# Kernel tuning notes

Measured on AMD Instinct MI355X. Metric: run time of the kernel, lower is better.

## Reference

```python
import jax, jax.numpy as jnp
import numpy as np

N_NODES = 100_000
N_EDGES = 1_600_000
NODE_FEATURES = 22


def setup_inputs() -> dict:
    key = jax.random.key(0)
    ks = jax.random.split(key, 10)
    s = 0.1
    x = jax.random.normal(ks[0], (N_NODES, NODE_FEATURES), dtype=jnp.float32)
    edge_index = jax.random.randint(ks[1], (2, N_EDGES), 0, N_NODES, dtype=jnp.int64)
    return {
        "x": x,
        "edge_index": edge_index,
        "W_embed": jax.random.normal(ks[2], (NODE_FEATURES, 32), jnp.float32) * s,
        "b_embed": jax.random.normal(ks[3], (32,), jnp.float32) * s,
        "W1": jax.random.normal(ks[4], (32, 32), jnp.float32) * s,
        "b1": jax.random.normal(ks[5], (32,), jnp.float32) * s,
        "W2": jax.random.normal(ks[6], (64, 32), jnp.float32) * s,
        "b2": jax.random.normal(ks[7], (32,), jnp.float32) * s,
        "W_pred": jax.random.normal(ks[8], (64, 1), jnp.float32) * s,
        "b_pred": jax.random.normal(ks[9], (1,), jnp.float32) * s,
    }


def gcn_conv(h, src, dst, deg_inv_sqrt, W, b, num_nodes):
    """PyG GCNConv: h' = scatter_add(norm_ij * (h W)[src] -> dst) + b.
    src/dst already include self-loops; deg_inv_sqrt precomputed on dst."""
    h = h @ W  # [N, out]
    norm = deg_inv_sqrt[src] * deg_inv_sqrt[dst]  # [E]
    msg = h[src] * norm[:, None]  # gather + normalize
    out = jax.ops.segment_sum(msg, dst, num_segments=num_nodes)  # scatter-add
    return out + b


def reference(x, edge_index, W_embed, b_embed, W1, b1, W2, b2, W_pred, b_pred):
    n = x.shape[0]
    loop = jnp.arange(n, dtype=edge_index.dtype)
    src = jnp.concatenate([edge_index[0], loop])  # add self-loops
    dst = jnp.concatenate([edge_index[1], loop])
    deg = jax.ops.segment_sum(jnp.ones_like(src, dtype=x.dtype), dst, num_segments=n)
    deg_inv_sqrt = jnp.where(deg > 0, jax.lax.rsqrt(jnp.maximum(deg, 1.0)), 0.0)

    h = x @ W_embed + b_embed  # MLP_embed
    # dropout is identity at eval time
    h0 = h
    h = gcn_conv(h, src, dst, deg_inv_sqrt, W1, b1, n)
    h = jax.nn.relu(h)
    h = jnp.concatenate([h, h0], axis=1)  # [N, 64]
    h = gcn_conv(h, src, dst, deg_inv_sqrt, W2, b2, n)
    h = jax.nn.relu(h)
    h = jnp.concatenate([h, h0], axis=1)  # [N, 64]
    delta = h @ W_pred + b_pred  # [N, 1]
    out = jax.nn.relu(delta + x[:, 1:2])
    return out
```

## Files before the change

### kernel.cpp

```cpp
#include <hip/hip_runtime.h>
#include <hip/hip_bf16.h>

#define NF 22
#define H  32
#define BSH 8
#define CAP 8192
#define CHUNK 2048

__device__ __forceinline__ float bflo(unsigned int v) { return __uint_as_float(v << 16); }
__device__ __forceinline__ float bfhi(unsigned int v) { return __uint_as_float(v & 0xffff0000u); }

__global__ void init_cur(int* __restrict__ cursor, int NB) {
    int i = blockIdx.x * blockDim.x + threadIdx.x;
    if (i < NB) cursor[i] = i * CAP;
}

__global__ __launch_bounds__(256) void bin_edges(
    const int* __restrict__ src, const int* __restrict__ dst,
    int* __restrict__ cursor, int* __restrict__ binned, int E, int NB)
{
    __shared__ int lh[512];
    __shared__ int lcur[512];
    int tid = threadIdx.x;
    for (int j = tid; j < NB; j += 256) lh[j] = 0;
    __syncthreads();
    int e0 = blockIdx.x * CHUNK;
    int ee = min(e0 + CHUNK, E);
    for (int i = e0 + tid; i < ee; i += 256) atomicAdd(&lh[dst[i] >> BSH], 1);
    __syncthreads();
    for (int j = tid; j < NB; j += 256) {
        int c = lh[j];
        if (c) lcur[j] = atomicAdd(&cursor[j], c);
    }
    __syncthreads();
    for (int i = e0 + tid; i < ee; i += 256) {
        int d = dst[i];
        int p = atomicAdd(&lcur[d >> BSH], 1);
        binned[p] = (src[i] << BSH) | (d & 255);
    }
}

__global__ __launch_bounds__(1024) void bucket_csr(
    const int* __restrict__ cursor, const int* __restrict__ binned,
    int* __restrict__ rowptr, int* __restrict__ rowcnt, int* __restrict__ sorted_src,
    float* __restrict__ dis, int N)
{
    __shared__ int cnt[256];
    __shared__ int s[256];
    __shared__ int lcur[256];
    int b = blockIdx.x, tid = threadIdx.x;
    int bn = b << BSH;
    if (tid < 256) cnt[tid] = 0;
    __syncthreads();
    int es = b * CAP, ee = cursor[b];
    for (int i = es + tid; i < ee; i += 1024) atomicAdd(&cnt[binned[i] & 255], 1);
    __syncthreads();
    int v = 0;
    if (tid < 256) { v = cnt[tid]; s[tid] = v; }
    __syncthreads();
    for (int off = 1; off < 256; off <<= 1) {
        int t = 0;
        if (tid < 256 && tid >= off) t = s[tid - off];
        __syncthreads();
        if (tid < 256) s[tid] += t;
        __syncthreads();
    }
    if (tid < 256) {
        int ex = s[tid] - v;
        lcur[tid] = ex;
        int n = bn + tid;
        if (n < N) {
            rowptr[n] = es + ex;
            rowcnt[n] = v;
            dis[n] = rsqrtf((float)(v + 1));
        }
    }
    __syncthreads();
    for (int i = es + tid; i < ee; i += 1024) {
        int e = binned[i];
        int p = atomicAdd(&lcur[e & 255], 1);
        sorted_src[es + p] = e >> BSH;
    }
}

__global__ __launch_bounds__(256) void embed_g1(
    const float* __restrict__ x, const float* __restrict__ We,
    const float* __restrict__ be, const float* __restrict__ W1,
    const float* __restrict__ dis, float* __restrict__ h0,
    __hip_bfloat16* __restrict__ g, int N)
{
    __shared__ float sWe[NF * H];
    __shared__ float sW1[H * H];
    __shared__ float sbe[H];
    __shared__ float sx[8][NF];
    __shared__ float sh[8][H];

    int tid = threadIdx.x;
    for (int j = tid; j < NF * H; j += 256) sWe[j] = We[j];
    for (int j = tid; j < H * H; j += 256) sW1[j] = W1[j];
    if (tid < H) sbe[tid] = be[tid];

    int grp = tid >> 5, t = tid & 31;
    int node = blockIdx.x * 8 + grp;
    int nodec = node < N ? node : N - 1;
    if (t < NF) sx[grp][t] = x[(size_t)nodec * NF + t];
    __syncthreads();

    float h = sbe[t];
#pragma unroll
    for (int k = 0; k < NF; k++) h += sx[grp][k] * sWe[k * H + t];
    sh[grp][t] = h;
    __syncthreads();

    float gv = 0.f;
#pragma unroll
    for (int k = 0; k < H; k++) gv += sh[grp][k] * sW1[k * H + t];
    gv *= dis[nodec];

    if (node < N) {
        size_t o = (size_t)node * H + t;
        h0[o] = h;
        g[o] = __float2bfloat16(gv);
    }
}

__global__ __launch_bounds__(256) void agg_mid(
    const int* __restrict__ rowptr, const int* __restrict__ rowcnt,
    const int* __restrict__ sorted_src,
    const __hip_bfloat16* __restrict__ g_in, const float* __restrict__ h0,
    const float* __restrict__ dis, const float* __restrict__ W2,
    const float* __restrict__ b1, __hip_bfloat16* __restrict__ g_out, int N)
{
    __shared__ float sW2[2 * H * H];
    __shared__ float srow[16][2 * H];

    int tid = threadIdx.x;
    for (int j = tid; j < 2 * H * H; j += 256) sW2[j] = W2[j];

    int grp = tid >> 4, lane = tid & 15;
    int node = blockIdx.x * 16 + grp;
    int nodec = node < N ? node : N - 1;

    const unsigned int* gv = (const unsigned int*)g_in;
    unsigned int sv = gv[(size_t)nodec * 16 + lane];
    float ax = bflo(sv), ay = bfhi(sv);

    int start = rowptr[nodec];
    int end = start + rowcnt[nodec];
    int i = start;
    for (; i + 7 < end; i += 8) {
        int s0 = sorted_src[i],     s1 = sorted_src[i + 1];
        int s2 = sorted_src[i + 2], s3 = sorted_src[i + 3];
        int s4 = sorted_src[i + 4], s5 = sorted_src[i + 5];
        int s6 = sorted_src[i + 6], s7 = sorted_src[i + 7];
        unsigned int v0 = gv[(size_t)s0 * 16 + lane], v1 = gv[(size_t)s1 * 16 + lane];
        unsigned int v2 = gv[(size_t)s2 * 16 + lane], v3 = gv[(size_t)s3 * 16 + lane];
        unsigned int v4 = gv[(size_t)s4 * 16 + lane], v5 = gv[(size_t)s5 * 16 + lane];
        unsigned int v6 = gv[(size_t)s6 * 16 + lane], v7 = gv[(size_t)s7 * 16 + lane];
        ax += bflo(v0) + bflo(v1) + bflo(v2) + bflo(v3)
            + bflo(v4) + bflo(v5) + bflo(v6) + bflo(v7);
        ay += bfhi(v0) + bfhi(v1) + bfhi(v2) + bfhi(v3)
            + bfhi(v4) + bfhi(v5) + bfhi(v6) + bfhi(v7);
    }
    for (; i + 3 < end; i += 4) {
        int s0 = sorted_src[i],     s1 = sorted_src[i + 1];
        int s2 = sorted_src[i + 2], s3 = sorted_src[i + 3];
        unsigned int v0 = gv[(size_t)s0 * 16 + lane], v1 = gv[(size_t)s1 * 16 + lane];
        unsigned int v2 = gv[(size_t)s2 * 16 + lane], v3 = gv[(size_t)s3 * 16 + lane];
        ax += bflo(v0) + bflo(v1) + bflo(v2) + bflo(v3);
        ay += bfhi(v0) + bfhi(v1) + bfhi(v2) + bfhi(v3);
    }
    for (; i < end; i++) {
        unsigned int v = gv[(size_t)sorted_src[i] * 16 + lane];
        ax += bflo(v); ay += bfhi(v);
    }

    float di = dis[nodec];
    float2 bb = ((const float2*)b1)[lane];
    float r0 = fmaxf(di * ax + bb.x, 0.f);
    float r1 = fmaxf(di * ay + bb.y, 0.f);
    float2 hh = ((const float2*)h0)[(size_t)nodec * 16 + lane];
    srow[grp][2 * lane]         = r0;
    srow[grp][2 * lane + 1]     = r1;
    srow[grp][H + 2 * lane]     = hh.x;
    srow[grp][H + 2 * lane + 1] = hh.y;
    __syncthreads();

    const float2* sW2v = (const float2*)sW2;
    float o0 = 0.f, o1 = 0.f;
#pragma unroll
    for (int k = 0; k < 2 * H; k++) {
        float rv = srow[grp][k];
        float2 w = sW2v[k * 16 + lane];
        o0 += rv * w.x;
        o1 += rv * w.y;
    }
    o0 *= di; o1 *= di;

    if (node < N) {
        __hip_bfloat162 p;
        p.x = __float2bfloat16(o0);
        p.y = __float2bfloat16(o1);
        ((__hip_bfloat162*)g_out)[(size_t)node * 16 + lane] = p;
    }
}

__global__ __launch_bounds__(256) void agg_final(
    const int* __restrict__ rowptr, const int* __restrict__ rowcnt,
    const int* __restrict__ sorted_src,
    const __hip_bfloat16* __restrict__ g_in, const float* __restrict__ h0,
    const float* __restrict__ dis, const float* __restrict__ b2,
    const float* __restrict__ Wp, const float* __restrict__ bp,
    const float* __restrict__ x, float* __restrict__ out, int N)
{
    int gid = blockIdx.x * blockDim.x + threadIdx.x;
    int node = gid >> 4;
    if (node >= N) return;
    int lane = gid & 15;

    const unsigned int* gv = (const unsigned int*)g_in;
    unsigned int sv = gv[(size_t)node * 16 + lane];
    float ax = bflo(sv), ay = bfhi(sv);

    int start = rowptr[node];
    int end = start + rowcnt[node];
    int i = start;
    for (; i + 7 < end; i += 8) {
        int s0 = sorted_src[i],     s1 = sorted_src[i + 1];
        int s2 = sorted_src[i + 2], s3 = sorted_src[i + 3];
        int s4 = sorted_src[i + 4], s5 = sorted_src[i + 5];
        int s6 = sorted_src[i + 6], s7 = sorted_src[i + 7];
        unsigned int v0 = gv[(size_t)s0 * 16 + lane], v1 = gv[(size_t)s1 * 16 + lane];
        unsigned int v2 = gv[(size_t)s2 * 16 + lane], v3 = gv[(size_t)s3 * 16 + lane];
        unsigned int v4 = gv[(size_t)s4 * 16 + lane], v5 = gv[(size_t)s5 * 16 + lane];
        unsigned int v6 = gv[(size_t)s6 * 16 + lane], v7 = gv[(size_t)s7 * 16 + lane];
        ax += bflo(v0) + bflo(v1) + bflo(v2) + bflo(v3)
            + bflo(v4) + bflo(v5) + bflo(v6) + bflo(v7);
        ay += bfhi(v0) + bfhi(v1) + bfhi(v2) + bfhi(v3)
            + bfhi(v4) + bfhi(v5) + bfhi(v6) + bfhi(v7);
    }
    for (; i + 3 < end; i += 4) {
        int s0 = sorted_src[i],     s1 = sorted_src[i + 1];
        int s2 = sorted_src[i + 2], s3 = sorted_src[i + 3];
        unsigned int v0 = gv[(size_t)s0 * 16 + lane], v1 = gv[(size_t)s1 * 16 + lane];
        unsigned int v2 = gv[(size_t)s2 * 16 + lane], v3 = gv[(size_t)s3 * 16 + lane];
        ax += bflo(v0) + bflo(v1) + bflo(v2) + bflo(v3);
        ay += bfhi(v0) + bfhi(v1) + bfhi(v2) + bfhi(v3);
    }
    for (; i < end; i++) {
        unsigned int v = gv[(size_t)sorted_src[i] * 16 + lane];
        ax += bflo(v); ay += bfhi(v);
    }

    float di = dis[node];
    float2 b2v = ((const float2*)b2)[lane];
    float2 wpa = ((const float2*)Wp)[lane];
    float2 wpb = ((const float2*)Wp)[16 + lane];
    float2 hh = ((const float2*)h0)[(size_t)node * 16 + lane];
    float v = fmaxf(di * ax + b2v.x, 0.f) * wpa.x
            + fmaxf(di * ay + b2v.y, 0.f) * wpa.y
            + hh.x * wpb.x + hh.y * wpb.y;
#pragma unroll
    for (int off = 8; off > 0; off >>= 1) v += __shfl_down(v, off, 16);
    if (lane == 0) out[node] = fmaxf(v + bp[0] + x[(size_t)node * NF + 1], 0.f);
}

extern "C" void kernel_launch(void* const* d_in, const int* in_sizes, int n_in,
                              void* d_out, int out_size, void* d_ws, size_t ws_size,
                              hipStream_t stream) {
    const float* x  = (const float*)d_in[0];
    const int*   ei = (const int*)d_in[1];
    const float* We = (const float*)d_in[2];
    const float* be = (const float*)d_in[3];
    const float* W1 = (const float*)d_in[4];
    const float* b1 = (const float*)d_in[5];
    const float* W2 = (const float*)d_in[6];
    const float* b2 = (const float*)d_in[7];
    const float* Wp = (const float*)d_in[8];
    const float* bp = (const float*)d_in[9];
    float* out = (float*)d_out;

    const int N = in_sizes[0] / NF;
    const int E = in_sizes[1] / 2;
    const int* src = ei;
    const int* dst = ei + E;
    const int NB = (N + 255) >> BSH;
    const int nchunk = (E + CHUNK - 1) / CHUNK;

    size_t Np  = ((size_t)N + 127) & ~(size_t)127;
    size_t NHp = ((size_t)N * H + 127) & ~(size_t)127;
    float* ws  = (float*)d_ws;
    float* dis = ws;
    float* h0  = dis + Np;
    __hip_bfloat16* g1 = (__hip_bfloat16*)(h0 + NHp);
    __hip_bfloat16* g2 = g1 + NHp;
    int* cursor     = (int*)(g2 + NHp);
    int* rowptr     = cursor + 512;
    int* rowcnt     = rowptr + Np;
    int* binned     = rowcnt + Np;
    int* sorted_src = binned + (size_t)NB * CAP;

    init_cur<<<2, 256, 0, stream>>>(cursor, NB);
    bin_edges<<<nchunk, 256, 0, stream>>>(src, dst, cursor, binned, E, NB);
    bucket_csr<<<NB, 1024, 0, stream>>>(cursor, binned, rowptr, rowcnt, sorted_src, dis, N);

    embed_g1<<<(N + 7) / 8, 256, 0, stream>>>(x, We, be, W1, dis, h0, g1, N);
    agg_mid<<<(N + 15) / 16, 256, 0, stream>>>(rowptr, rowcnt, sorted_src, g1, h0, dis, W2, b1, g2, N);
    agg_final<<<((size_t)N * 16 + 255) / 256, 256, 0, stream>>>(rowptr, rowcnt, sorted_src, g2, h0, dis, b2, Wp, bp, x, out, N);
}
```

Baseline: 222.9 us.

## Precompute h0 projections in embed kernel instead of storing h0

```diff
diff --git a/kernel.cpp b/kernel.cpp
--- a/kernel.cpp
+++ b/kernel.cpp
@@ -86,19 +86,25 @@
 __global__ __launch_bounds__(256) void embed_g1(
     const float* __restrict__ x, const float* __restrict__ We,
     const float* __restrict__ be, const float* __restrict__ W1,
-    const float* __restrict__ dis, float* __restrict__ h0,
-    __hip_bfloat16* __restrict__ g, int N)
+    const float* __restrict__ W2, const float* __restrict__ Wp,
+    const float* __restrict__ bp, const float* __restrict__ dis,
+    __hip_bfloat16* __restrict__ g, __hip_bfloat16* __restrict__ y2,
+    float* __restrict__ hp, int N)
 {
     __shared__ float sWe[NF * H];
     __shared__ float sW1[H * H];
+    __shared__ float sW2b[H * H];
     __shared__ float sbe[H];
+    __shared__ float sWpb[H];
     __shared__ float sx[8][NF];
     __shared__ float sh[8][H];
 
     int tid = threadIdx.x;
     for (int j = tid; j < NF * H; j += 256) sWe[j] = We[j];
     for (int j = tid; j < H * H; j += 256) sW1[j] = W1[j];
+    for (int j = tid; j < H * H; j += 256) sW2b[j] = W2[H * H + j];
     if (tid < H) sbe[tid] = be[tid];
+    if (tid >= H && tid < 2 * H) sWpb[tid - H] = Wp[tid];
 
     int grp = tid >> 5, t = tid & 31;
     int node = blockIdx.x * 8 + grp;
@@ -112,30 +118,40 @@
     sh[grp][t] = h;
     __syncthreads();
 
-    float gv = 0.f;
-#pragma unroll
-    for (int k = 0; k < H; k++) gv += sh[grp][k] * sW1[k * H + t];
-    gv *= dis[nodec];
+    float di = dis[nodec];
+    float gv = 0.f, yv = 0.f;
+#pragma unroll
+    for (int k = 0; k < H; k++) {
+        float hv = sh[grp][k];
+        gv += hv * sW1[k * H + t];
+        yv += hv * sW2b[k * H + t];
+    }
+    gv *= di;
+
+    float pv = h * sWpb[t];
+#pragma unroll
+    for (int off = 16; off > 0; off >>= 1) pv += __shfl_down(pv, off, 32);
 
     if (node < N) {
         size_t o = (size_t)node * H + t;
-        h0[o] = h;
         g[o] = __float2bfloat16(gv);
+        y2[o] = __float2bfloat16(yv);
+        if (t == 0) hp[node] = pv + bp[0] + sx[grp][1];
     }
 }
 
 __global__ __launch_bounds__(256) void agg_mid(
     const int* __restrict__ rowptr, const int* __restrict__ rowcnt,
     const int* __restrict__ sorted_src,
-    const __hip_bfloat16* __restrict__ g_in, const float* __restrict__ h0,
+    const __hip_bfloat16* __restrict__ g_in, const __hip_bfloat16* __restrict__ y2,
     const float* __restrict__ dis, const float* __restrict__ W2,
     const float* __restrict__ b1, __hip_bfloat16* __restrict__ g_out, int N)
 {
-    __shared__ float sW2[2 * H * H];
-    __shared__ float srow[16][2 * H];
+    __shared__ float sW2[H * H];
+    __shared__ float srow[16][33];
 
     int tid = threadIdx.x;
-    for (int j = tid; j < 2 * H * H; j += 256) sW2[j] = W2[j];
+    for (int j = tid; j < H * H; j += 256) sW2[j] = W2[j];
 
     int grp = tid >> 4, lane = tid & 15;
     int node = blockIdx.x * 16 + grp;
@@ -177,25 +193,22 @@
 
     float di = dis[nodec];
     float2 bb = ((const float2*)b1)[lane];
-    float r0 = fmaxf(di * ax + bb.x, 0.f);
-    float r1 = fmaxf(di * ay + bb.y, 0.f);
-    float2 hh = ((const float2*)h0)[(size_t)nodec * 16 + lane];
-    srow[grp][2 * lane]         = r0;
-    srow[grp][2 * lane + 1]     = r1;
-    srow[grp][H + 2 * lane]     = hh.x;
-    srow[grp][H + 2 * lane + 1] = hh.y;
+    srow[grp][2 * lane]     = fmaxf(di * ax + bb.x, 0.f);
+    srow[grp][2 * lane + 1] = fmaxf(di * ay + bb.y, 0.f);
     __syncthreads();
 
     const float2* sW2v = (const float2*)sW2;
     float o0 = 0.f, o1 = 0.f;
 #pragma unroll
-    for (int k = 0; k < 2 * H; k++) {
+    for (int k = 0; k < H; k++) {
         float rv = srow[grp][k];
         float2 w = sW2v[k * 16 + lane];
         o0 += rv * w.x;
         o1 += rv * w.y;
     }
-    o0 *= di; o1 *= di;
+    unsigned int yv = ((const unsigned int*)y2)[(size_t)nodec * 16 + lane];
+    o0 = di * (o0 + bflo(yv));
+    o1 = di * (o1 + bfhi(yv));
 
     if (node < N) {
         __hip_bfloat162 p;
@@ -208,10 +221,9 @@
 __global__ __launch_bounds__(256) void agg_final(
     const int* __restrict__ rowptr, const int* __restrict__ rowcnt,
     const int* __restrict__ sorted_src,
-    const __hip_bfloat16* __restrict__ g_in, const float* __restrict__ h0,
+    const __hip_bfloat16* __restrict__ g_in, const float* __restrict__ hp,
     const float* __restrict__ dis, const float* __restrict__ b2,
-    const float* __restrict__ Wp, const float* __restrict__ bp,
-    const float* __restrict__ x, float* __restrict__ out, int N)
+    const float* __restrict__ Wp, float* __restrict__ out, int N)
 {
     int gid = blockIdx.x * blockDim.x + threadIdx.x;
     int node = gid >> 4;
@@ -255,14 +267,11 @@
     float di = dis[node];
     float2 b2v = ((const float2*)b2)[lane];
     float2 wpa = ((const float2*)Wp)[lane];
-    float2 wpb = ((const float2*)Wp)[16 + lane];
-    float2 hh = ((const float2*)h0)[(size_t)node * 16 + lane];
     float v = fmaxf(di * ax + b2v.x, 0.f) * wpa.x
-            + fmaxf(di * ay + b2v.y, 0.f) * wpa.y
-            + hh.x * wpb.x + hh.y * wpb.y;
+            + fmaxf(di * ay + b2v.y, 0.f) * wpa.y;
 #pragma unroll
     for (int off = 8; off > 0; off >>= 1) v += __shfl_down(v, off, 16);
-    if (lane == 0) out[node] = fmaxf(v + bp[0] + x[(size_t)node * NF + 1], 0.f);
+    if (lane == 0) out[node] = fmaxf(v + hp[node], 0.f);
 }
 
 extern "C" void kernel_launch(void* const* d_in, const int* in_sizes, int n_in,
@@ -291,10 +300,11 @@
     size_t NHp = ((size_t)N * H + 127) & ~(size_t)127;
     float* ws  = (float*)d_ws;
     float* dis = ws;
-    float* h0  = dis + Np;
-    __hip_bfloat16* g1 = (__hip_bfloat16*)(h0 + NHp);
+    float* hp  = dis + Np;
+    __hip_bfloat16* g1 = (__hip_bfloat16*)(hp + Np);
     __hip_bfloat16* g2 = g1 + NHp;
-    int* cursor     = (int*)(g2 + NHp);
+    __hip_bfloat16* y2 = g2 + NHp;
+    int* cursor     = (int*)(y2 + NHp);
     int* rowptr     = cursor + 512;
     int* rowcnt     = rowptr + Np;
     int* binned     = rowcnt + Np;
@@ -304,7 +314,7 @@
     bin_edges<<<nchunk, 256, 0, stream>>>(src, dst, cursor, binned, E, NB);
     bucket_csr<<<NB, 1024, 0, stream>>>(cursor, binned, rowptr, rowcnt, sorted_src, dis, N);
 
-    embed_g1<<<(N + 7) / 8, 256, 0, stream>>>(x, We, be, W1, dis, h0, g1, N);
-    agg_mid<<<(N + 15) / 16, 256, 0, stream>>>(rowptr, rowcnt, sorted_src, g1, h0, dis, W2, b1, g2, N);
-    agg_final<<<((size_t)N * 16 + 255) / 256, 256, 0, stream>>>(rowptr, rowcnt, sorted_src, g2, h0, dis, b2, Wp, bp, x, out, N);
-}
+    embed_g1<<<(N + 7) / 8, 256, 0, stream>>>(x, We, be, W1, W2, Wp, bp, dis, g1, y2, hp, N);
+    agg_mid<<<(N + 15) / 16, 256, 0, stream>>>(rowptr, rowcnt, sorted_src, g1, y2, dis, W2, b1, g2, N);
+    agg_final<<<((size_t)N * 16 + 255) / 256, 256, 0, stream>>>(rowptr, rowcnt, sorted_src, g2, hp, dis, b2, Wp, out, N);
+}
```

After: 223.6 us. No clear change (+0.3%).
